# Kernel optimization log

Hardware: AMD Instinct MI355X
Metric: run time of the kernel (lower is better)

Reference implementation:

```python
import jax, jax.numpy as jnp
import numpy as np


def setup_inputs() -> dict:
    key = jax.random.key(0)
    B, S, N, H, GS = 2, 4096, 16, 64, 128
    k0, k1, k2, k3, k4 = jax.random.split(key, 5)
    # per-modality [start, end) segment boundaries (3 modalities)
    modal_index = np.array([[0, 1024], [1024, 3072], [3072, 4096]], dtype=np.int64)
    return {
        "modal_index": modal_index,
        "query_layer": jax.random.normal(k0, (B, S, N, H), jnp.float32),
        "key_layer": jax.random.normal(k1, (B, S, N, H), jnp.float32),
        "value_layer": jax.random.normal(k2, (B, S, N, H), jnp.float32),
        "local_attention_mask": jnp.zeros((B, 1, 1, S), jnp.float32),
        "global_attention_mask_is_not_None": 1,
        "global_k": jax.random.normal(k3, (B, N, GS, H), jnp.float32),
        "global_v": jax.random.normal(k4, (B, N, GS, H), jnp.float32),
        "global_selection_padding_mask_zeros": jnp.zeros((B, 1, 1, GS), jnp.float32),
    }


def reference(modal_index, query_layer, key_layer, value_layer,
              local_attention_mask, global_attention_mask_is_not_None,
              global_k, global_v, global_selection_padding_mask_zeros):
    # [B,S,N,H] -> [B,N,S,H] (matches permute(0,2,1,3) in the torch module)
    q = jnp.transpose(query_layer, (0, 2, 1, 3))
    k = jnp.transpose(key_layer, (0, 2, 1, 3))
    v = jnp.transpose(value_layer, (0, 2, 1, 3))
    H = q.shape[-1]
    gs = global_k.shape[2]
    scale = 1.0 / jnp.sqrt(jnp.asarray(H, q.dtype))
    segments = [(int(a), int(b)) for a, b in np.asarray(modal_index)]

    outs = []
    for st, en in segments:  # small fixed modality count, not a data-dim loop
        qs = q[:, :, st:en]            # [B,N,s,H]
        ks = k[:, :, st:en]
        vs = v[:, :, st:en]
        # local scores within the segment + additive local key mask slice
        scores_l = jnp.einsum('bnqh,bnkh->bnqk', qs, ks) * scale \
                   + local_attention_mask[:, :, :, st:en]        # [B,N,s,s]
        if global_attention_mask_is_not_None:
            scores_g = jnp.einsum('bnqh,bngh->bnqg', qs, global_k) * scale \
                       + global_selection_padding_mask_zeros      # [B,N,s,gs]
            probs = jax.nn.softmax(jnp.concatenate([scores_g, scores_l], axis=-1), axis=-1)
            ctx = jnp.einsum('bnqg,bngh->bnqh', probs[..., :gs], global_v) \
                  + jnp.einsum('bnqk,bnkh->bnqh', probs[..., gs:], vs)
        else:
            ctx = jnp.einsum('bnqk,bnkh->bnqh', jax.nn.softmax(scores_l, axis=-1), vs)
        outs.append(ctx)

    out = jnp.concatenate(outs, axis=2)           # [B,N,S,H]
    return jnp.transpose(out, (0, 2, 1, 3))       # back to [B,S,N,H]
```

## Files before the change

### kernel.cpp

```cpp
#include <hip/hip_runtime.h>

typedef unsigned int u32;
typedef unsigned short u16;
typedef __attribute__((ext_vector_type(8))) short bf16x8;
typedef __attribute__((ext_vector_type(4))) float f32x4;

#define BB 2
#define SS 4096
#define NN 16
#define HH 64
#define GSZ 128
#define QT 128
#define KT 64
#define PITCH 70
#define SCALE 0.125f

__device__ __forceinline__ u16 f2bf(float f){
    u32 x = __float_as_uint(f);
    return (u16)((x + 0x7fffu + ((x >> 16) & 1u)) >> 16);
}
__device__ __forceinline__ u32 pk2(float a, float b){
    return (u32)f2bf(a) | ((u32)f2bf(b) << 16);
}

__global__ __launch_bounds__(256) void prep_bf16(
    const float* __restrict__ K, const float* __restrict__ V,
    const float* __restrict__ GK, const float* __restrict__ GV,
    u16* __restrict__ ws, size_t NK, size_t NG)
{
    size_t idx = ((size_t)blockIdx.x * 256 + threadIdx.x) * 8;
    const float* src;
    if      (idx < NK)          src = K  + idx;
    else if (idx < 2*NK)        src = V  + (idx - NK);
    else if (idx < 2*NK + NG)   src = GK + (idx - 2*NK);
    else                        src = GV + (idx - 2*NK - NG);
    float4 a = *(const float4*)src;
    float4 b = *(const float4*)(src + 4);
    uint4 o = make_uint4(pk2(a.x,a.y), pk2(a.z,a.w), pk2(b.x,b.y), pk2(b.z,b.w));
    *(uint4*)(ws + idx) = o;
}

template<int PRE>
__global__ __launch_bounds__(512, 4) void mmattn_mfma(
    const void* __restrict__ modal_index, int nseg,
    const float* __restrict__ Q,  const float* __restrict__ Kf, const float* __restrict__ Vf,
    const float* __restrict__ LM, const int* __restrict__ hasg_p,
    const float* __restrict__ GKf, const float* __restrict__ GVf, const float* __restrict__ GM,
    const u16* __restrict__ Kb, const u16* __restrict__ Vb,
    const u16* __restrict__ GKb, const u16* __restrict__ GVb,
    float* __restrict__ Out)
{
    __shared__ u16 Klds[KT * PITCH];
    __shared__ u16 Vt  [HH * PITCH];
    __shared__ u16 Pl  [8 * 16 * PITCH];

    const int bid = blockIdx.x;
    const int xcd = bid & 7, ii = bid >> 3;
    const int p   = xcd * 4 + (ii >> 5);
    const int b   = p >> 4, n = p & 15;
    const int q0  = (ii & 31) * QT;

    const int tid = threadIdx.x;
    const int wid = tid >> 6, lane = tid & 63;
    const int lr  = lane & 15, lg = lane >> 4;
    const int srow = tid >> 3;
    const int sc8  = (tid & 7) * 8;

    const int*       p32 = (const int*)modal_index;
    const long long* p64 = (const long long*)modal_index;
    const bool is32 = (p32[2 * nseg - 1] == SS);
    int st = 0, en = SS;
    for (int i = 0; i < nseg; ++i) {
        int a = is32 ? p32[2*i]   : (int)p64[2*i];
        int c = is32 ? p32[2*i+1] : (int)p64[2*i+1];
        if (q0 >= a && q0 < c) { st = a; en = c; }
    }

    bf16x8 qa0, qa1;
    {
        const float* qp = Q + (((size_t)(b * SS + q0 + wid * 16 + lr)) * NN + n) * HH + lg * 8;
        float4 f0 = *(const float4*)(qp);
        float4 f1 = *(const float4*)(qp + 4);
        float4 f2 = *(const float4*)(qp + 32);
        float4 f3 = *(const float4*)(qp + 36);
        union { u32 w[4]; bf16x8 v; } ua, ub;
        ua.w[0]=pk2(f0.x,f0.y); ua.w[1]=pk2(f0.z,f0.w); ua.w[2]=pk2(f1.x,f1.y); ua.w[3]=pk2(f1.z,f1.w);
        ub.w[0]=pk2(f2.x,f2.y); ub.w[1]=pk2(f2.z,f2.w); ub.w[2]=pk2(f3.x,f3.y); ub.w[3]=pk2(f3.z,f3.w);
        qa0 = ua.v; qa1 = ub.v;
    }

    f32x4 o[4];
    #pragma unroll
    for (int hb = 0; hb < 4; ++hb) { o[hb][0]=0.f; o[hb][1]=0.f; o[hb][2]=0.f; o[hb][3]=0.f; }
    float m[4] = {-1e30f,-1e30f,-1e30f,-1e30f};
    float l[4] = {0.f,0.f,0.f,0.f};

    u16* Plw = &Pl[wid * 16 * PITCH];

    auto tile = [&](const void* kb, const void* vb, size_t rs, const float* mp) {
        if constexpr (PRE) {
            const u16* kp = (const u16*)kb + (size_t)srow * rs + sc8;
            *(uint4*)&Klds[srow * PITCH + sc8] = *(const uint4*)kp;
            const u16* vp = (const u16*)vb + (size_t)srow * rs + sc8;
            uint4 w = *(const uint4*)vp;
            u16 vv[8] = {(u16)w.x,(u16)(w.x>>16),(u16)w.y,(u16)(w.y>>16),
                         (u16)w.z,(u16)(w.z>>16),(u16)w.w,(u16)(w.w>>16)};
            #pragma unroll
            for (int j = 0; j < 8; ++j) Vt[(sc8 + j) * PITCH + srow] = vv[j];
        } else {
            const float* kp = (const float*)kb + (size_t)srow * rs + sc8;
            float4 ka = *(const float4*)kp;
            float4 kc = *(const float4*)(kp + 4);
            *(uint4*)&Klds[srow * PITCH + sc8] =
                make_uint4(pk2(ka.x,ka.y), pk2(ka.z,ka.w), pk2(kc.x,kc.y), pk2(kc.z,kc.w));
            const float* vp = (const float*)vb + (size_t)srow * rs + sc8;
            float4 va = *(const float4*)vp;
            float4 vc = *(const float4*)(vp + 4);
            float vv[8] = {va.x,va.y,va.z,va.w, vc.x,vc.y,vc.z,vc.w};
            #pragma unroll
            for (int j = 0; j < 8; ++j) Vt[(sc8 + j) * PITCH + srow] = f2bf(vv[j]);
        }
        __syncthreads();

        float mk[4];
        #pragma unroll
        for (int cb = 0; cb < 4; ++cb) mk[cb] = mp[cb * 16 + lr];

        f32x4 s[4];
        #pragma unroll
        for (int cb = 0; cb < 4; ++cb) {
            const bf16x8 kb0 = *(const bf16x8*)&Klds[(cb*16 + lr) * PITCH + lg*8];
            const bf16x8 kb1 = *(const bf16x8*)&Klds[(cb*16 + lr) * PITCH + 32 + lg*8];
            f32x4 acc; acc[0]=0.f; acc[1]=0.f; acc[2]=0.f; acc[3]=0.f;
            acc = __builtin_amdgcn_mfma_f32_16x16x32_bf16(qa0, kb0, acc, 0, 0, 0);
            acc = __builtin_amdgcn_mfma_f32_16x16x32_bf16(qa1, kb1, acc, 0, 0, 0);
            s[cb] = acc;
        }

        float cr[4];
        #pragma unroll
        for (int r = 0; r < 4; ++r) {
            float s0 = s[0][r]*SCALE + mk[0];
            float s1 = s[1][r]*SCALE + mk[1];
            float s2 = s[2][r]*SCALE + mk[2];
            float s3 = s[3][r]*SCALE + mk[3];
            float mx = fmaxf(fmaxf(s0, s1), fmaxf(s2, s3));
            mx = fmaxf(mx, __shfl_xor(mx, 1));
            mx = fmaxf(mx, __shfl_xor(mx, 2));
            mx = fmaxf(mx, __shfl_xor(mx, 4));
            mx = fmaxf(mx, __shfl_xor(mx, 8));
            float nm = fmaxf(m[r], mx);
            float c_ = __expf(m[r] - nm);
            m[r] = nm;
            float p0 = __expf(s0 - nm), p1 = __expf(s1 - nm);
            float p2 = __expf(s2 - nm), p3 = __expf(s3 - nm);
            float rsum = (p0 + p1) + (p2 + p3);
            rsum += __shfl_xor(rsum, 1);
            rsum += __shfl_xor(rsum, 2);
            rsum += __shfl_xor(rsum, 4);
            rsum += __shfl_xor(rsum, 8);
            l[r] = l[r] * c_ + rsum;
            cr[r] = c_;
            u16* pw = &Plw[(lg * 4 + r) * PITCH + lr];
            pw[0]  = f2bf(p0); pw[16] = f2bf(p1);
            pw[32] = f2bf(p2); pw[48] = f2bf(p3);
        }
        #pragma unroll
        for (int hb = 0; hb < 4; ++hb) {
            o[hb][0]*=cr[0]; o[hb][1]*=cr[1]; o[hb][2]*=cr[2]; o[hb][3]*=cr[3];
        }

        const bf16x8 pa0 = *(const bf16x8*)&Plw[lr * PITCH + lg*8];
        const bf16x8 pa1 = *(const bf16x8*)&Plw[lr * PITCH + 32 + lg*8];
        #pragma unroll
        for (int hb = 0; hb < 4; ++hb) {
            const bf16x8 vb0 = *(const bf16x8*)&Vt[(hb*16 + lr) * PITCH + lg*8];
            const bf16x8 vb1 = *(const bf16x8*)&Vt[(hb*16 + lr) * PITCH + 32 + lg*8];
            o[hb] = __builtin_amdgcn_mfma_f32_16x16x32_bf16(pa0, vb0, o[hb], 0, 0, 0);
            o[hb] = __builtin_amdgcn_mfma_f32_16x16x32_bf16(pa1, vb1, o[hb], 0, 0, 0);
        }
        __syncthreads();
    };

    if (*hasg_p) {
        const float* gmb = GM + (size_t)b * GSZ;
        if constexpr (PRE) {
            const u16* gkb = GKb + ((size_t)(b * NN + n)) * GSZ * HH;
            const u16* gvb = GVb + ((size_t)(b * NN + n)) * GSZ * HH;
            tile(gkb,           gvb,           HH, gmb);
            tile(gkb + 64*HH,   gvb + 64*HH,   HH, gmb + 64);
        } else {
            const float* gkb = GKf + ((size_t)(b * NN + n)) * GSZ * HH;
            const float* gvb = GVf + ((size_t)(b * NN + n)) * GSZ * HH;
            tile(gkb,           gvb,           HH, gmb);
            tile(gkb + 64*HH,   gvb + 64*HH,   HH, gmb + 64);
        }
    }
    {
        const float* lmb = LM + (size_t)b * SS;
        for (int k0 = st; k0 < en; k0 += KT) {
            if constexpr (PRE) {
                tile(Kb + (((size_t)(b * SS + k0)) * NN + n) * HH,
                     Vb + (((size_t)(b * SS + k0)) * NN + n) * HH,
                     (size_t)NN * HH, lmb + k0);
            } else {
                tile(Kf + (((size_t)(b * SS + k0)) * NN + n) * HH,
                     Vf + (((size_t)(b * SS + k0)) * NN + n) * HH,
                     (size_t)NN * HH, lmb + k0);
            }
        }
    }

    float inv[4] = {1.f/l[0], 1.f/l[1], 1.f/l[2], 1.f/l[3]};
    #pragma unroll
    for (int hb = 0; hb < 4; ++hb) {
        #pragma unroll
        for (int r = 0; r < 4; ++r) {
            const int qrow = q0 + wid * 16 + lg * 4 + r;
            Out[(((size_t)(b * SS + qrow)) * NN + n) * HH + hb * 16 + lr] = o[hb][r] * inv[r];
        }
    }
}

extern "C" void kernel_launch(void* const* d_in, const int* in_sizes, int n_in,
                              void* d_out, int out_size, void* d_ws, size_t ws_size,
                              hipStream_t stream)
{
    const void* modal = d_in[0];
    const int   nseg  = in_sizes[0] / 2;
    const float* Q  = (const float*)d_in[1];
    const float* K  = (const float*)d_in[2];
    const float* V  = (const float*)d_in[3];
    const float* LM = (const float*)d_in[4];
    const int*   HG = (const int*)d_in[5];
    const float* GK = (const float*)d_in[6];
    const float* GV = (const float*)d_in[7];
    const float* GM = (const float*)d_in[8];
    float* Out = (float*)d_out;

    const size_t NK = (size_t)BB * SS * NN * HH;
    const size_t NG = (size_t)BB * NN * GSZ * HH;
    const size_t need = (2*NK + 2*NG) * sizeof(u16);

    const int nblk = (SS / QT) * NN * BB;

    if (d_ws && ws_size >= need) {
        u16* wsp = (u16*)d_ws;
        const size_t tot8 = (2*NK + 2*NG) / 8;
        prep_bf16<<<(int)(tot8 / 256), 256, 0, stream>>>(K, V, GK, GV, wsp, NK, NG);
        mmattn_mfma<1><<<nblk, 512, 0, stream>>>(modal, nseg, Q, K, V, LM, HG, GK, GV, GM,
                                                 wsp, wsp + NK, wsp + 2*NK, wsp + 2*NK + NG, Out);
    } else {
        mmattn_mfma<0><<<nblk, 512, 0, stream>>>(modal, nseg, Q, K, V, LM, HG, GK, GV, GM,
                                                 nullptr, nullptr, nullptr, nullptr, Out);
    }
}
```

Measured before the change: 435.6 us.

## Double-buffer K/V tiles with register prefetch, lazy softmax rescale, smaller Q tile

Splits the key loop into a single unified tile sequence covering global tiles then segment tiles, and prefetches the next tile's K/V into registers while the current tile is computed from one of two LDS buffers. The Q tile drops to 64 rows with 256-thread blocks. The online softmax now skips the max reduction and rescaling unless some row max grows past a threshold, and defers the row-sum shuffle reduction to the end. It trades more registers and LDS for less global-load latency and fewer shuffles per tile; smaller Q tiles mean more K/V reloads across blocks.

```diff
diff --git a/kernel.cpp b/kernel.cpp
--- a/kernel.cpp
+++ b/kernel.cpp
@@ -10,10 +10,11 @@
 #define NN 16
 #define HH 64
 #define GSZ 128
-#define QT 128
+#define QT 64
 #define KT 64
 #define PITCH 70
 #define SCALE 0.125f
+#define THR 8.0f
 
 __device__ __forceinline__ u16 f2bf(float f){
     u32 x = __float_as_uint(f);
@@ -36,12 +37,11 @@
     else                        src = GV + (idx - 2*NK - NG);
     float4 a = *(const float4*)src;
     float4 b = *(const float4*)(src + 4);
-    uint4 o = make_uint4(pk2(a.x,a.y), pk2(a.z,a.w), pk2(b.x,b.y), pk2(b.z,b.w));
-    *(uint4*)(ws + idx) = o;
+    *(uint4*)(ws + idx) = make_uint4(pk2(a.x,a.y), pk2(a.z,a.w), pk2(b.x,b.y), pk2(b.z,b.w));
 }
 
 template<int PRE>
-__global__ __launch_bounds__(512, 4) void mmattn_mfma(
+__global__ __launch_bounds__(256, 3) void mmattn_mfma(
     const void* __restrict__ modal_index, int nseg,
     const float* __restrict__ Q,  const float* __restrict__ Kf, const float* __restrict__ Vf,
     const float* __restrict__ LM, const int* __restrict__ hasg_p,
@@ -50,21 +50,21 @@
     const u16* __restrict__ GKb, const u16* __restrict__ GVb,
     float* __restrict__ Out)
 {
-    __shared__ u16 Klds[KT * PITCH];
-    __shared__ u16 Vt  [HH * PITCH];
-    __shared__ u16 Pl  [8 * 16 * PITCH];
+    __shared__ u16 Kl[2][KT * PITCH];
+    __shared__ u16 Vt[2][HH * PITCH];
+    __shared__ u16 Pl[4 * 16 * PITCH];
 
     const int bid = blockIdx.x;
     const int xcd = bid & 7, ii = bid >> 3;
-    const int p   = xcd * 4 + (ii >> 5);
-    const int b   = p >> 4, n = p & 15;
-    const int q0  = (ii & 31) * QT;
+    const int pr  = xcd * 4 + (ii >> 6);
+    const int b   = pr >> 4, n = pr & 15;
+    const int q0  = (ii & 63) * QT;
 
     const int tid = threadIdx.x;
     const int wid = tid >> 6, lane = tid & 63;
     const int lr  = lane & 15, lg = lane >> 4;
-    const int srow = tid >> 3;
-    const int sc8  = (tid & 7) * 8;
+    const int rp  = tid >> 3;
+    const int g8  = (tid & 7) * 8;
 
     const int*       p32 = (const int*)modal_index;
     const long long* p64 = (const long long*)modal_index;
@@ -75,6 +75,8 @@
         int c = is32 ? p32[2*i+1] : (int)p64[2*i+1];
         if (q0 >= a && q0 < c) { st = a; en = c; }
     }
+    const int ng = (*hasg_p) ? 2 : 0;
+    const int nt = ng + (en - st) / KT;
 
     bf16x8 qa0, qa1;
     {
@@ -94,123 +96,156 @@
     for (int hb = 0; hb < 4; ++hb) { o[hb][0]=0.f; o[hb][1]=0.f; o[hb][2]=0.f; o[hb][3]=0.f; }
     float m[4] = {-1e30f,-1e30f,-1e30f,-1e30f};
     float l[4] = {0.f,0.f,0.f,0.f};
-
     u16* Plw = &Pl[wid * 16 * PITCH];
 
-    auto tile = [&](const void* kb, const void* vb, size_t rs, const float* mp) {
+    auto ptrs = [&](int t, const void*& kp, const void*& vp, size_t& rs, const float*& mp) {
+        if (t < ng) {
+            size_t off = ((size_t)(b * NN + n)) * GSZ * HH + (size_t)t * KT * HH;
+            if constexpr (PRE) { kp = GKb + off; vp = GVb + off; }
+            else               { kp = GKf + off; vp = GVf + off; }
+            rs = HH; mp = GM + (size_t)b * GSZ + t * KT;
+        } else {
+            int k0 = st + (t - ng) * KT;
+            size_t off = (((size_t)(b * SS + k0)) * NN + n) * HH;
+            if constexpr (PRE) { kp = Kb + off; vp = Vb + off; }
+            else               { kp = Kf + off; vp = Vf + off; }
+            rs = (size_t)NN * HH; mp = LM + (size_t)b * SS + k0;
+        }
+    };
+
+    uint4 kr0, kr1, vr0, vr1;
+    float4 ka0,ka1,kb0_,kb1_, va0,va1,vb0_,vb1_;
+
+    auto issue = [&](int t) {
+        const void *kp, *vp; size_t rs; const float* mp_;
+        ptrs(t, kp, vp, rs, mp_);
         if constexpr (PRE) {
-            const u16* kp = (const u16*)kb + (size_t)srow * rs + sc8;
-            *(uint4*)&Klds[srow * PITCH + sc8] = *(const uint4*)kp;
-            const u16* vp = (const u16*)vb + (size_t)srow * rs + sc8;
-            uint4 w = *(const uint4*)vp;
-            u16 vv[8] = {(u16)w.x,(u16)(w.x>>16),(u16)w.y,(u16)(w.y>>16),
-                         (u16)w.z,(u16)(w.z>>16),(u16)w.w,(u16)(w.w>>16)};
-            #pragma unroll
-            for (int j = 0; j < 8; ++j) Vt[(sc8 + j) * PITCH + srow] = vv[j];
+            const u16* k0p = (const u16*)kp + (size_t)(2*rp)   * rs + g8;
+            const u16* k1p = (const u16*)kp + (size_t)(2*rp+1) * rs + g8;
+            const u16* v0p = (const u16*)vp + (size_t)(2*rp)   * rs + g8;
+            const u16* v1p = (const u16*)vp + (size_t)(2*rp+1) * rs + g8;
+            kr0 = *(const uint4*)k0p; kr1 = *(const uint4*)k1p;
+            vr0 = *(const uint4*)v0p; vr1 = *(const uint4*)v1p;
         } else {
-            const float* kp = (const float*)kb + (size_t)srow * rs + sc8;
-            float4 ka = *(const float4*)kp;
-            float4 kc = *(const float4*)(kp + 4);
-            *(uint4*)&Klds[srow * PITCH + sc8] =
-                make_uint4(pk2(ka.x,ka.y), pk2(ka.z,ka.w), pk2(kc.x,kc.y), pk2(kc.z,kc.w));
-            const float* vp = (const float*)vb + (size_t)srow * rs + sc8;
-            float4 va = *(const float4*)vp;
-            float4 vc = *(const float4*)(vp + 4);
-            float vv[8] = {va.x,va.y,va.z,va.w, vc.x,vc.y,vc.z,vc.w};
-            #pragma unroll
-            for (int j = 0; j < 8; ++j) Vt[(sc8 + j) * PITCH + srow] = f2bf(vv[j]);
-        }
-        __syncthreads();
-
+            const float* k0p = (const float*)kp + (size_t)(2*rp)   * rs + g8;
+            const float* k1p = (const float*)kp + (size_t)(2*rp+1) * rs + g8;
+            const float* v0p = (const float*)vp + (size_t)(2*rp)   * rs + g8;
+            const float* v1p = (const float*)vp + (size_t)(2*rp+1) * rs + g8;
+            ka0 = *(const float4*)k0p; ka1 = *(const float4*)(k0p + 4);
+            kb0_= *(const float4*)k1p; kb1_= *(const float4*)(k1p + 4);
+            va0 = *(const float4*)v0p; va1 = *(const float4*)(v0p + 4);
+            vb0_= *(const float4*)v1p; vb1_= *(const float4*)(v1p + 4);
+        }
+    };
+
+    auto commit = [&](int bi) {
+        if constexpr (PRE) {
+            *(uint4*)&Kl[bi][(2*rp)   * PITCH + g8] = kr0;
+            *(uint4*)&Kl[bi][(2*rp+1) * PITCH + g8] = kr1;
+            union { uint4 v; u16 h[8]; } a, c;
+            a.v = vr0; c.v = vr1;
+            #pragma unroll
+            for (int j = 0; j < 8; ++j) {
+                u32 w = (u32)a.h[j] | ((u32)c.h[j] << 16);
+                *(u32*)&Vt[bi][(g8 + j) * PITCH + 2*rp] = w;
+            }
+        } else {
+            *(uint4*)&Kl[bi][(2*rp)   * PITCH + g8] =
+                make_uint4(pk2(ka0.x,ka0.y), pk2(ka0.z,ka0.w), pk2(ka1.x,ka1.y), pk2(ka1.z,ka1.w));
+            *(uint4*)&Kl[bi][(2*rp+1) * PITCH + g8] =
+                make_uint4(pk2(kb0_.x,kb0_.y), pk2(kb0_.z,kb0_.w), pk2(kb1_.x,kb1_.y), pk2(kb1_.z,kb1_.w));
+            float va[8] = {va0.x,va0.y,va0.z,va0.w, va1.x,va1.y,va1.z,va1.w};
+            float vc[8] = {vb0_.x,vb0_.y,vb0_.z,vb0_.w, vb1_.x,vb1_.y,vb1_.z,vb1_.w};
+            #pragma unroll
+            for (int j = 0; j < 8; ++j) {
+                u32 w = (u32)f2bf(va[j]) | ((u32)f2bf(vc[j]) << 16);
+                *(u32*)&Vt[bi][(g8 + j) * PITCH + 2*rp] = w;
+            }
+        }
+    };
+
+    issue(0); commit(0); __syncthreads();
+    int cur = 0;
+    for (int t = 0; t < nt; ++t) {
+        if (t + 1 < nt) issue(t + 1);
+
+        const void *kp_, *vp_; size_t rs_; const float* mp_;
+        ptrs(t, kp_, vp_, rs_, mp_);
         float mk[4];
         #pragma unroll
-        for (int cb = 0; cb < 4; ++cb) mk[cb] = mp[cb * 16 + lr];
+        for (int cb = 0; cb < 4; ++cb) mk[cb] = mp_[cb * 16 + lr];
 
         f32x4 s[4];
         #pragma unroll
         for (int cb = 0; cb < 4; ++cb) {
-            const bf16x8 kb0 = *(const bf16x8*)&Klds[(cb*16 + lr) * PITCH + lg*8];
-            const bf16x8 kb1 = *(const bf16x8*)&Klds[(cb*16 + lr) * PITCH + 32 + lg*8];
+            const bf16x8 kf0 = *(const bf16x8*)&Kl[cur][(cb*16 + lr) * PITCH + lg*8];
+            const bf16x8 kf1 = *(const bf16x8*)&Kl[cur][(cb*16 + lr) * PITCH + 32 + lg*8];
             f32x4 acc; acc[0]=0.f; acc[1]=0.f; acc[2]=0.f; acc[3]=0.f;
-            acc = __builtin_amdgcn_mfma_f32_16x16x32_bf16(qa0, kb0, acc, 0, 0, 0);
-            acc = __builtin_amdgcn_mfma_f32_16x16x32_bf16(qa1, kb1, acc, 0, 0, 0);
+            acc = __builtin_amdgcn_mfma_f32_16x16x32_bf16(qa0, kf0, acc, 0, 0, 0);
+            acc = __builtin_amdgcn_mfma_f32_16x16x32_bf16(qa1, kf1, acc, 0, 0, 0);
             s[cb] = acc;
         }
 
-        float cr[4];
+        float sv[4][4], pm[4];
         #pragma unroll
         for (int r = 0; r < 4; ++r) {
-            float s0 = s[0][r]*SCALE + mk[0];
-            float s1 = s[1][r]*SCALE + mk[1];
-            float s2 = s[2][r]*SCALE + mk[2];
-            float s3 = s[3][r]*SCALE + mk[3];
-            float mx = fmaxf(fmaxf(s0, s1), fmaxf(s2, s3));
-            mx = fmaxf(mx, __shfl_xor(mx, 1));
-            mx = fmaxf(mx, __shfl_xor(mx, 2));
-            mx = fmaxf(mx, __shfl_xor(mx, 4));
-            mx = fmaxf(mx, __shfl_xor(mx, 8));
-            float nm = fmaxf(m[r], mx);
-            float c_ = __expf(m[r] - nm);
-            m[r] = nm;
-            float p0 = __expf(s0 - nm), p1 = __expf(s1 - nm);
-            float p2 = __expf(s2 - nm), p3 = __expf(s3 - nm);
-            float rsum = (p0 + p1) + (p2 + p3);
-            rsum += __shfl_xor(rsum, 1);
-            rsum += __shfl_xor(rsum, 2);
-            rsum += __shfl_xor(rsum, 4);
-            rsum += __shfl_xor(rsum, 8);
-            l[r] = l[r] * c_ + rsum;
-            cr[r] = c_;
+            #pragma unroll
+            for (int cb = 0; cb < 4; ++cb) sv[r][cb] = s[cb][r] * SCALE + mk[cb];
+            pm[r] = fmaxf(fmaxf(sv[r][0], sv[r][1]), fmaxf(sv[r][2], sv[r][3]));
+        }
+        int lok = (pm[0] <= m[0] + THR) & (pm[1] <= m[1] + THR) &
+                  (pm[2] <= m[2] + THR) & (pm[3] <= m[3] + THR);
+        if (!__all(lok)) {
+            #pragma unroll
+            for (int r = 0; r < 4; ++r) {
+                float mx = pm[r];
+                mx = fmaxf(mx, __shfl_xor(mx, 1));
+                mx = fmaxf(mx, __shfl_xor(mx, 2));
+                mx = fmaxf(mx, __shfl_xor(mx, 4));
+                mx = fmaxf(mx, __shfl_xor(mx, 8));
+                float nm = fmaxf(m[r], mx);
+                float c_ = __expf(m[r] - nm);
+                l[r] *= c_;
+                o[0][r] *= c_; o[1][r] *= c_; o[2][r] *= c_; o[3][r] *= c_;
+                m[r] = nm;
+            }
+        }
+        #pragma unroll
+        for (int r = 0; r < 4; ++r) {
+            float p0 = __expf(sv[r][0] - m[r]);
+            float p1 = __expf(sv[r][1] - m[r]);
+            float p2 = __expf(sv[r][2] - m[r]);
+            float p3 = __expf(sv[r][3] - m[r]);
+            l[r] += (p0 + p1) + (p2 + p3);
             u16* pw = &Plw[(lg * 4 + r) * PITCH + lr];
             pw[0]  = f2bf(p0); pw[16] = f2bf(p1);
             pw[32] = f2bf(p2); pw[48] = f2bf(p3);
         }
-        #pragma unroll
-        for (int hb = 0; hb < 4; ++hb) {
-            o[hb][0]*=cr[0]; o[hb][1]*=cr[1]; o[hb][2]*=cr[2]; o[hb][3]*=cr[3];
-        }
 
         const bf16x8 pa0 = *(const bf16x8*)&Plw[lr * PITCH + lg*8];
         const bf16x8 pa1 = *(const bf16x8*)&Plw[lr * PITCH + 32 + lg*8];
         #pragma unroll
         for (int hb = 0; hb < 4; ++hb) {
-            const bf16x8 vb0 = *(const bf16x8*)&Vt[(hb*16 + lr) * PITCH + lg*8];
-            const bf16x8 vb1 = *(const bf16x8*)&Vt[(hb*16 + lr) * PITCH + 32 + lg*8];
-            o[hb] = __builtin_amdgcn_mfma_f32_16x16x32_bf16(pa0, vb0, o[hb], 0, 0, 0);
-            o[hb] = __builtin_amdgcn_mfma_f32_16x16x32_bf16(pa1, vb1, o[hb], 0, 0, 0);
-        }
+            const bf16x8 vf0 = *(const bf16x8*)&Vt[cur][(hb*16 + lr) * PITCH + lg*8];
+            const bf16x8 vf1 = *(const bf16x8*)&Vt[cur][(hb*16 + lr) * PITCH + 32 + lg*8];
+            o[hb] = __builtin_amdgcn_mfma_f32_16x16x32_bf16(pa0, vf0, o[hb], 0, 0, 0);
+            o[hb] = __builtin_amdgcn_mfma_f32_16x16x32_bf16(pa1, vf1, o[hb], 0, 0, 0);
+        }
+
+        if (t + 1 < nt) commit(cur ^ 1);
         __syncthreads();
-    };
-
-    if (*hasg_p) {
-        const float* gmb = GM + (size_t)b * GSZ;
-        if constexpr (PRE) {
-            const u16* gkb = GKb + ((size_t)(b * NN + n)) * GSZ * HH;
-            const u16* gvb = GVb + ((size_t)(b * NN + n)) * GSZ * HH;
-            tile(gkb,           gvb,           HH, gmb);
-            tile(gkb + 64*HH,   gvb + 64*HH,   HH, gmb + 64);
-        } else {
-            const float* gkb = GKf + ((size_t)(b * NN + n)) * GSZ * HH;
-            const float* gvb = GVf + ((size_t)(b * NN + n)) * GSZ * HH;
-            tile(gkb,           gvb,           HH, gmb);
-            tile(gkb + 64*HH,   gvb + 64*HH,   HH, gmb + 64);
-        }
-    }
-    {
-        const float* lmb = LM + (size_t)b * SS;
-        for (int k0 = st; k0 < en; k0 += KT) {
-            if constexpr (PRE) {
-                tile(Kb + (((size_t)(b * SS + k0)) * NN + n) * HH,
-                     Vb + (((size_t)(b * SS + k0)) * NN + n) * HH,
-                     (size_t)NN * HH, lmb + k0);
-            } else {
-                tile(Kf + (((size_t)(b * SS + k0)) * NN + n) * HH,
-                     Vf + (((size_t)(b * SS + k0)) * NN + n) * HH,
-                     (size_t)NN * HH, lmb + k0);
-            }
-        }
-    }
-
+        cur ^= 1;
+    }
+
+    #pragma unroll
+    for (int r = 0; r < 4; ++r) {
+        float t_ = l[r];
+        t_ += __shfl_xor(t_, 1);
+        t_ += __shfl_xor(t_, 2);
+        t_ += __shfl_xor(t_, 4);
+        t_ += __shfl_xor(t_, 8);
+        l[r] = t_;
+    }
     float inv[4] = {1.f/l[0], 1.f/l[1], 1.f/l[2], 1.f/l[3]};
     #pragma unroll
     for (int hb = 0; hb < 4; ++hb) {
@@ -241,17 +276,16 @@
     const size_t NK = (size_t)BB * SS * NN * HH;
     const size_t NG = (size_t)BB * NN * GSZ * HH;
     const size_t need = (2*NK + 2*NG) * sizeof(u16);
-
     const int nblk = (SS / QT) * NN * BB;
 
     if (d_ws && ws_size >= need) {
         u16* wsp = (u16*)d_ws;
         const size_t tot8 = (2*NK + 2*NG) / 8;
         prep_bf16<<<(int)(tot8 / 256), 256, 0, stream>>>(K, V, GK, GV, wsp, NK, NG);
-        mmattn_mfma<1><<<nblk, 512, 0, stream>>>(modal, nseg, Q, K, V, LM, HG, GK, GV, GM,
+        mmattn_mfma<1><<<nblk, 256, 0, stream>>>(modal, nseg, Q, K, V, LM, HG, GK, GV, GM,
                                                  wsp, wsp + NK, wsp + 2*NK, wsp + 2*NK + NG, Out);
     } else {
-        mmattn_mfma<0><<<nblk, 512, 0, stream>>>(modal, nseg, Q, K, V, LM, HG, GK, GV, GM,
+        mmattn_mfma<0><<<nblk, 256, 0, stream>>>(modal, nseg, Q, K, V, LM, HG, GK, GV, GM,
                                                  nullptr, nullptr, nullptr, nullptr, Out);
     }
 }
```

Measured after the change: 359.5 us. 1.21x faster.
